# Kernel optimization log

Hardware: AMD Instinct MI355X
Metric: run time of the kernel (lower is better)

## Reference

```python
import jax, jax.numpy as jnp
import numpy as np

B, T, CNN, HW = 512, 256, 512, 7
V, H = 37, 8  # vocab_size, hidden_size


def setup_inputs() -> dict:
    key = jax.random.key(0)
    ks = jax.random.split(key, 10)
    s = 0.1
    return {
        "features": jax.random.normal(ks[0], (B, CNN, HW, HW), jnp.float32),
        "captions": jax.random.normal(ks[1], (B, T, V), jnp.float32),
        "W_in": jax.random.normal(ks[2], (V, CNN), jnp.float32) * s,
        "b_in": jax.random.normal(ks[3], (V,), jnp.float32) * s,
        "W_ih": jax.random.normal(ks[4], (4 * H, V), jnp.float32) * s,
        "W_hh": jax.random.normal(ks[5], (4 * H, H), jnp.float32) * s,
        "b_ih": jax.random.normal(ks[6], (4 * H,), jnp.float32) * s,
        "b_hh": jax.random.normal(ks[7], (4 * H,), jnp.float32) * s,
        "W_out": jax.random.normal(ks[8], (V, H), jnp.float32) * s,
        "b_out": jax.random.normal(ks[9], (V,), jnp.float32) * s,
    }


def reference(features, captions, W_in, b_in, W_ih, W_hh, b_ih, b_hh, W_out, b_out):
    # AdaptiveAvgPool2d(1) + flatten + fc_in -> [B, V]
    feat = features.mean(axis=(2, 3)) @ W_in.T + b_in
    # input at t=0 is feat, at t>0 is captions[:, t-1]; build [T, B, V] sequence
    xs = jnp.concatenate([feat[None], jnp.swapaxes(captions, 0, 1)[:-1]], axis=0)

    def step(carry, x):
        h, c = carry
        gates = x @ W_ih.T + b_ih + h @ W_hh.T + b_hh  # [B, 4H]
        i, f, g, o = jnp.split(gates, 4, axis=1)  # PyTorch LSTMCell gate order
        i = jax.nn.sigmoid(i)
        f = jax.nn.sigmoid(f)
        g = jnp.tanh(g)
        o = jax.nn.sigmoid(o)
        c = f * c + i * g
        h = o * jnp.tanh(c)
        out = jax.nn.softmax(h @ W_out.T + b_out, axis=1)  # [B, V]
        return (h, c), out

    h0 = jnp.zeros((feat.shape[0], W_hh.shape[1]), feat.dtype)
    c0 = jnp.zeros_like(h0)
    _, outs = jax.lax.scan(step, (h0, c0), xs)  # outs: [T, B, V]
    return jnp.swapaxes(outs, 0, 1)  # [B, T, V]
```

## Files before the change

### kernel.cpp

```cpp
#include <hip/hip_runtime.h>
#include <math.h>

#define BB   512
#define TT   256
#define CNNC 512
#define VV   37
#define HH   8
#define G4   32
#define CH   16
#define NCH  (TT / CH)
#define CHW  (CH * 128)

#define L2E 1.4426950408889634f

typedef float f4_t __attribute__((ext_vector_type(4)));
typedef float f2_t __attribute__((ext_vector_type(2)));

template <int CTRL>
__device__ __forceinline__ float dpp_f(float x) {
    int r = __builtin_amdgcn_update_dpp(0, __float_as_int(x), CTRL, 0xF, 0xF, true);
    return __int_as_float(r);
}

__device__ __forceinline__ float rcp_f(float x) { return __builtin_amdgcn_rcpf(x); }
__device__ __forceinline__ float exp2_f(float x) { return __builtin_amdgcn_exp2f(x); }

__global__ __launch_bounds__(256) void k_feat(const float* __restrict__ features,
                                              const float* __restrict__ W_in,
                                              const float* __restrict__ b_in,
                                              float* __restrict__ featp) {
    __shared__ __align__(16) float raw[128 * 49];
    __shared__ float pooled[128];
    const int b = blockIdx.x, qt = blockIdx.y, tid = threadIdx.x;
    const f4_t* src =
        (const f4_t*)(features + (size_t)b * CNNC * 49 + qt * (128 * 49));
    f4_t* dst = (f4_t*)raw;
    for (int i = tid; i < 128 * 49 / 4; i += 256)
        dst[i] = __builtin_nontemporal_load(&src[i]);
    __syncthreads();
    if (tid < 128) {
        const float* p = raw + tid * 49;
        float s = 0.f;
        #pragma unroll
        for (int i = 0; i < 49; ++i) s += p[i];
        pooled[tid] = s;
    }
    __syncthreads();
    const int v = tid >> 2, pp = tid & 3;
    if (v < VV) {
        const float* w = W_in + v * CNNC + qt * 128 + pp * 32;
        const float* q = pooled + pp * 32;
        float s = 0.f;
        #pragma unroll
        for (int i = 0; i < 32; ++i) s += q[i] * w[i];
        s += __shfl_xor(s, 1);
        s += __shfl_xor(s, 2);
        if (pp == 0)
            featp[(qt * BB + b) * VV + v] =
                s * (1.f / 49.f) + (qt == 0 ? b_in[v] : 0.f);
    }
}

#define CAPS 1188
#define SOS  132
__global__ __launch_bounds__(256) void k_xproj(const float* __restrict__ captions,
                                               const float* __restrict__ W_ih,
                                               const float* __restrict__ b_ih,
                                               const float* __restrict__ b_hh,
                                               const float* __restrict__ featp,
                                               float* __restrict__ xproj) {
    __shared__ float W[G4 * VV];
    __shared__ float bias[G4];
    __shared__ float cap[4 * CAPS];
    __shared__ __align__(16) float so[32 * SOS];
    const int bg = blockIdx.x, tile = blockIdx.y;
    const int tid = threadIdx.x;
    for (int i = tid; i < G4 * VV; i += 256) W[i] = W_ih[i];
    if (tid < G4) bias[tid] = b_ih[tid] + b_hh[tid];

    const int t0 = tile * 32;
    const int start = (tile == 0) ? 0 : t0 - 1;
    for (int i = tid; i < 4 * 1184; i += 256) {
        const int s2 = i / 1184;
        const int off = i - s2 * 1184;
        cap[s2 * CAPS + off] = __builtin_nontemporal_load(
            &captions[((size_t)(bg * 4 + s2) * TT + start) * VV + off]);
    }
    __syncthreads();

    const int tl = tid >> 3;
    const int s  = (tid >> 1) & 3;
    const int r  = tid & 1;
    const int b  = bg * 4 + s;

    float xr[VV];
    if (tile == 0 && tl == 0) {
        #pragma unroll
        for (int v = 0; v < VV; ++v)
            xr[v] = featp[b * VV + v] + featp[(BB + b) * VV + v] +
                    featp[(2 * BB + b) * VV + v] + featp[(3 * BB + b) * VV + v];
    } else {
        const int lr = (tile == 0) ? tl - 1 : tl;
        const float* x = &cap[s * CAPS + lr * VV];
        #pragma unroll
        for (int v = 0; v < VV; ++v) xr[v] = x[v];
    }

    const int g0 = r * 16;
    float acc[16];
    #pragma unroll
    for (int g = 0; g < 16; ++g) acc[g] = bias[g0 + g];
    #pragma unroll
    for (int v = 0; v < VV; ++v) {
        const float xv = xr[v];
        #pragma unroll
        for (int g = 0; g < 16; ++g) acc[g] += xv * W[(g0 + g) * VV + v];
    }
    #pragma unroll
    for (int g = 0; g < 16; ++g) {
        const int gg = g0 + g;
        const float sc = (gg >= 16 && gg < 24) ? (-2.f * L2E) : (-L2E);
        const int word = ((gg & 15) * 4 + s) * 2 + (gg >> 4);
        so[tl * SOS + word] = acc[g] * sc;
    }
    __syncthreads();

    float* chunk = xproj + ((size_t)bg * TT + t0) * 128;
    for (int i = tid; i < 1024; i += 256) {
        const int t2 = i >> 5, rest = i & 31;
        f4_t val = *(const f4_t*)&so[t2 * SOS + rest * 4];
        *(f4_t*)&chunk[t2 * 128 + rest * 4] = val;
    }
}

#define TSTR 12
#define SSTR (CH * TSTR + 4)

#define STEP(cur, tl) do {                                                  \
    const float pA = cur[tl].x, pB = cur[tl].y;                             \
    const float ha0 = h;                                                    \
    const float ha1 = dpp_f<0x4E>(h);                                       \
    const float ha3 = dpp_f<0x141>(h);                                      \
    const float ha2 = dpp_f<0x4E>(ha3);                                     \
    const float ha7 = dpp_f<0x140>(h);                                      \
    const float ha4 = dpp_f<0x141>(ha7);                                    \
    const float ha5 = dpp_f<0x4E>(ha4);                                     \
    const float ha6 = dpp_f<0x1B>(ha7);                                     \
    float a0 = fmaf(wA[0], ha0, pA);                                        \
    a0 = fmaf(wA[1], ha1, a0);                                              \
    a0 = fmaf(wA[2], ha2, a0);                                              \
    a0 = fmaf(wA[3], ha3, a0);                                              \
    float a1 = wA[4] * ha4;                                                 \
    a1 = fmaf(wA[5], ha5, a1);                                              \
    a1 = fmaf(wA[6], ha6, a1);                                              \
    a1 = fmaf(wA[7], ha7, a1);                                              \
    const float npA = a0 + a1;                                              \
    float b0 = fmaf(wB[0], ha0, pB);                                        \
    b0 = fmaf(wB[1], ha1, b0);                                              \
    b0 = fmaf(wB[2], ha2, b0);                                              \
    b0 = fmaf(wB[3], ha3, b0);                                              \
    float b1 = wB[4] * ha4;                                                 \
    b1 = fmaf(wB[5], ha5, b1);                                              \
    b1 = fmaf(wB[6], ha6, b1);                                              \
    b1 = fmaf(wB[7], ha7, b1);                                              \
    const float npB = b0 + b1;                                              \
    const float eA = rcp_f(1.f + exp2_f(npA));         \
    const float uB = rcp_f(1.f + exp2_f(npB));     \
    const float gg = fmaf(-4.f * L2E, uB, 2.f * L2E);    \
    const float myU = r ? eA : eA * gg;           \
    const float otU = dpp_f<0xB1>(myU);                                     \
    const float fg  = r ? myU : otU;                                        \
    const float igg = r ? otU : myU;                                        \
    const float ogx = dpp_f<0xB1>(uB);                                      \
    const float og  = r ? uB : ogx;                                         \
    c = fmaf(fg, c, igg);                         \
    const float rv = rcp_f(1.f + exp2_f(c));                                \
    const float og2 = og + og;                                              \
    h = fmaf(og2, rv, -og);                                 \
    hsv[tl] = h;                                                            \
} while (0)

#define CHUNK(cur, nxt, it, pbuf) do {                                      \
    if ((it) + 1 < NCH) {                                                   \
        const f2_t* src = (const f2_t*)(xp + ((it) + 1) * CHW + roff2);     \
        _Pragma("unroll")                                                   \
        for (int tl = 0; tl < CH; ++tl) nxt[tl] = src[tl * 64];             \
        __builtin_amdgcn_sched_barrier(0);                                  \
    }                                                                       \
    _Pragma("unroll")                                                       \
    for (int tl = 0; tl < CH; ++tl) STEP(cur, tl);                          \
    if (r == 0) {                                                           \
        float* hb = &hst[((pbuf) * 4 + s4) * SSTR + j];                     \
        _Pragma("unroll")                                                   \
        for (int i = 0; i < CH; ++i) hb[i * TSTR] = hsv[i];                 \
    }                                                                       \
} while (0)

#define EMIT(pk) do {                                                       \
    const int os = lane >> 4, otl = lane & 15;                              \
    const float* hp = &hst[(((pk) & 1) * 4 + os) * SSTR + otl * TSTR];      \
    const f4_t h0 = *(const f4_t*)hp;                                       \
    const f4_t h1 = *(const f4_t*)(hp + 4);                                 \
    const f4_t* W4 = (const f4_t*)Wo;                                       \
    float z[VV];                                                            \
    float m = -1e30f;                                                       \
    _Pragma("unroll")                                                       \
    for (int v = 0; v < VV; ++v) {                                          \
        const f4_t w0 = W4[v * 2], w1 = W4[v * 2 + 1];                      \
        float sv = bo[v];                                                   \
        sv = fmaf(h0.x, w0.x, sv); sv = fmaf(h0.y, w0.y, sv);               \
        sv = fmaf(h0.z, w0.z, sv); sv = fmaf(h0.w, w0.w, sv);               \
        sv = fmaf(h1.x, w1.x, sv); sv = fmaf(h1.y, w1.y, sv);               \
        sv = fmaf(h1.z, w1.z, sv); sv = fmaf(h1.w, w1.w, sv);               \
        z[v] = sv;                                                          \
        m = fmaxf(m, sv);                                                   \
    }                                                                       \
    float sum = 0.f;                                                        \
    _Pragma("unroll")                                                       \
    for (int v = 0; v < VV; ++v) {                                          \
        z[v] = exp2_f((z[v] - m) * L2E);                                    \
        sum += z[v];                                                        \
    }                                                                       \
    const float rs = rcp_f(sum);                                            \
    const int ob = bg * 4 + os;                                             \
    const int ot = (pk) * CH + otl;                                         \
    float* op = out + ((size_t)ob * TT + ot) * VV;                          \
    _Pragma("unroll")                                                       \
    for (int v = 0; v < VV; ++v) op[v] = z[v] * rs;                         \
} while (0)

__global__ __launch_bounds__(128) void k_lstm(const float* __restrict__ W_hh,
                                              const float* __restrict__ xproj,
                                              const float* __restrict__ W_out,
                                              const float* __restrict__ b_out,
                                              float* __restrict__ out) {
    __shared__ __align__(16) float hst[2 * 4 * SSTR];
    __shared__ __align__(16) float Wo[VV * HH];
    __shared__ float bo[VV];

    const int tid  = threadIdx.x;
    const int wv   = tid >> 6;
    const int lane = tid & 63;
    const int bg   = blockIdx.x;
    const float* xp = xproj + (size_t)bg * (TT * 128);

    const int s4 = lane >> 4;
    const int q  = lane & 15;
    const int j  = q >> 1;
    const int r  = q & 1;
    const int rowA  = r * 8 + j;
    const int roff2 = (rowA * 4 + s4) * 2;

    f2_t cA[CH], cB[CH];
    float hsv[CH];
    float wA[HH], wB[HH];

    if (wv == 0) {
        const int rowB = 16 + rowA;
        const float scA = -L2E;
        const float scB = r ? -L2E : (-2.f * L2E);
        #pragma unroll
        for (int m = 0; m < HH; ++m) {
            wA[m] = scA * W_hh[rowA * HH + (j ^ m)];
            wB[m] = scB * W_hh[rowB * HH + (j ^ m)];
        }
        const f2_t* src = (const f2_t*)(xp + roff2);
        #pragma unroll
        for (int tl = 0; tl < CH; ++tl) cA[tl] = src[tl * 64];
    } else {
        for (int i = lane; i < VV * HH; i += 64) Wo[i] = W_out[i];
        if (lane < VV) bo[lane] = b_out[lane];
    }

    float h = 0.f, c = 0.f;

    for (int ou = 0; ou < 9; ++ou) {
        {
            const int it = ou * 2;
            if (wv == 0) {
                if (it < NCH) CHUNK(cA, cB, it, 0);
            } else if (it >= 1 && it <= NCH) {
                EMIT(it - 1);
            }
            asm volatile("s_waitcnt lgkmcnt(0)" ::: "memory");
            __builtin_amdgcn_s_barrier();
            __builtin_amdgcn_sched_barrier(0);
        }
        {
            const int it = ou * 2 + 1;
            if (it <= NCH) {
                if (wv == 0) {
                    if (it < NCH) CHUNK(cB, cA, it, 1);
                } else {
                    EMIT(it - 1);
                }
                asm volatile("s_waitcnt lgkmcnt(0)" ::: "memory");
                __builtin_amdgcn_s_barrier();
                __builtin_amdgcn_sched_barrier(0);
            }
        }
    }
}

extern "C" void kernel_launch(void* const* d_in, const int* in_sizes, int n_in,
                              void* d_out, int out_size, void* d_ws, size_t ws_size,
                              hipStream_t stream) {
    const float* features = (const float*)d_in[0];
    const float* captions = (const float*)d_in[1];
    const float* W_in     = (const float*)d_in[2];
    const float* b_in     = (const float*)d_in[3];
    const float* W_ih     = (const float*)d_in[4];
    const float* W_hh     = (const float*)d_in[5];
    const float* b_ih     = (const float*)d_in[6];
    const float* b_hh     = (const float*)d_in[7];
    const float* W_out    = (const float*)d_in[8];
    const float* b_out    = (const float*)d_in[9];
    float* out = (float*)d_out;

    float* ws    = (float*)d_ws;
    float* featp = ws;
    float* xproj = ws + 81920;

    k_feat <<<dim3(BB, 4),  256, 0, stream>>>(features, W_in, b_in, featp);
    k_xproj<<<dim3(128, 8), 256, 0, stream>>>(captions, W_ih, b_ih, b_hh, featp, xproj);
    k_lstm <<<128,          128, 0, stream>>>(W_hh, xproj, W_out, b_out, out);
}
```

Baseline: 192.2 us.

## Map one LSTM hidden unit per lane with all four gates, 8 sequences per wave

The recurrent kernel now puts each hidden unit's four gates in a single lane, so no DPP exchange is needed between gate pairs. Each wave covers 8 sequences instead of 4, which halves the grid to 64 blocks and halves the chunk length. The xproj layout is rearranged so each lane reads one float4 per timestep. Softmax outputs are staged in shared memory and written with coalesced nontemporal vector stores. The trade-off is more serial arithmetic per lane on the recurrence critical path and fewer blocks to cover the GPU's compute units.

```diff
diff --git a/kernel.cpp b/kernel.cpp
--- a/kernel.cpp
+++ b/kernel.cpp
@@ -7,14 +7,13 @@
 #define VV   37
 #define HH   8
 #define G4   32
-#define CH   16
+#define CH   8
 #define NCH  (TT / CH)
-#define CHW  (CH * 128)
+#define CHW  (CH * 256)
 
 #define L2E 1.4426950408889634f
 
 typedef float f4_t __attribute__((ext_vector_type(4)));
-typedef float f2_t __attribute__((ext_vector_type(2)));
 
 template <int CTRL>
 __device__ __forceinline__ float dpp_f(float x) {
@@ -118,18 +117,20 @@
     }
     #pragma unroll
     for (int g = 0; g < 16; ++g) {
-        const int gg = g0 + g;
-        const float sc = (gg >= 16 && gg < 24) ? (-2.f * L2E) : (-L2E);
-        const int word = ((gg & 15) * 4 + s) * 2 + (gg >> 4);
+        const int gg   = g0 + g;
+        const int gate = gg >> 3;
+        const int j    = gg & 7;
+        const float sc = (gate == 2) ? (-2.f * L2E) : (-L2E);
+        const int word = s * 32 + j * 4 + gate;
         so[tl * SOS + word] = acc[g] * sc;
     }
     __syncthreads();
 
-    float* chunk = xproj + ((size_t)bg * TT + t0) * 128;
+    float* chunk = xproj + ((size_t)(bg >> 1) * TT + t0) * 256 + (bg & 1) * 128;
     for (int i = tid; i < 1024; i += 256) {
         const int t2 = i >> 5, rest = i & 31;
         f4_t val = *(const f4_t*)&so[t2 * SOS + rest * 4];
-        *(f4_t*)&chunk[t2 * 128 + rest * 4] = val;
+        *(f4_t*)&chunk[t2 * 256 + rest * 4] = val;
     }
 }
 
@@ -137,68 +138,75 @@
 #define SSTR (CH * TSTR + 4)
 
 #define STEP(cur, tl) do {                                                  \
-    const float pA = cur[tl].x, pB = cur[tl].y;                             \
+    const float pI = cur[tl].x, pF = cur[tl].y;                             \
+    const float pG = cur[tl].z, pO = cur[tl].w;                             \
     const float ha0 = h;                                                    \
-    const float ha1 = dpp_f<0x4E>(h);                                       \
-    const float ha3 = dpp_f<0x141>(h);                                      \
-    const float ha2 = dpp_f<0x4E>(ha3);                                     \
-    const float ha7 = dpp_f<0x140>(h);                                      \
-    const float ha4 = dpp_f<0x141>(ha7);                                    \
-    const float ha5 = dpp_f<0x4E>(ha4);                                     \
-    const float ha6 = dpp_f<0x1B>(ha7);                                     \
-    float a0 = fmaf(wA[0], ha0, pA);                                        \
-    a0 = fmaf(wA[1], ha1, a0);                                              \
-    a0 = fmaf(wA[2], ha2, a0);                                              \
-    a0 = fmaf(wA[3], ha3, a0);                                              \
-    float a1 = wA[4] * ha4;                                                 \
-    a1 = fmaf(wA[5], ha5, a1);                                              \
-    a1 = fmaf(wA[6], ha6, a1);                                              \
-    a1 = fmaf(wA[7], ha7, a1);                                              \
-    const float npA = a0 + a1;                                              \
-    float b0 = fmaf(wB[0], ha0, pB);                                        \
-    b0 = fmaf(wB[1], ha1, b0);                                              \
-    b0 = fmaf(wB[2], ha2, b0);                                              \
-    b0 = fmaf(wB[3], ha3, b0);                                              \
-    float b1 = wB[4] * ha4;                                                 \
-    b1 = fmaf(wB[5], ha5, b1);                                              \
-    b1 = fmaf(wB[6], ha6, b1);                                              \
-    b1 = fmaf(wB[7], ha7, b1);                                              \
-    const float npB = b0 + b1;                                              \
-    const float eA = rcp_f(1.f + exp2_f(npA));         \
-    const float uB = rcp_f(1.f + exp2_f(npB));     \
-    const float gg = fmaf(-4.f * L2E, uB, 2.f * L2E);    \
-    const float myU = r ? eA : eA * gg;           \
-    const float otU = dpp_f<0xB1>(myU);                                     \
-    const float fg  = r ? myU : otU;                                        \
-    const float igg = r ? otU : myU;                                        \
-    const float ogx = dpp_f<0xB1>(uB);                                      \
-    const float og  = r ? uB : ogx;                                         \
-    c = fmaf(fg, c, igg);                         \
+    const float ha1 = dpp_f<0xB1>(h);                                       \
+    const float ha2 = dpp_f<0x4E>(h);                                       \
+    const float ha3 = dpp_f<0x1B>(h);                                       \
+    const float ha7 = dpp_f<0x141>(h);                                      \
+    const float ha4 = dpp_f<0x1B>(ha7);                                     \
+    const float ha5 = dpp_f<0x4E>(ha7);                                     \
+    const float ha6 = dpp_f<0xB1>(ha7);                                     \
+    float iA = fmaf(wI[0], ha0, pI);                                        \
+    iA = fmaf(wI[1], ha1, iA); iA = fmaf(wI[2], ha2, iA);                   \
+    iA = fmaf(wI[3], ha3, iA);                                              \
+    float iB = wI[4] * ha4;                                                 \
+    iB = fmaf(wI[5], ha5, iB); iB = fmaf(wI[6], ha6, iB);                   \
+    iB = fmaf(wI[7], ha7, iB);                                              \
+    const float npI = iA + iB;                                              \
+    float fA = fmaf(wF[0], ha0, pF);                                        \
+    fA = fmaf(wF[1], ha1, fA); fA = fmaf(wF[2], ha2, fA);                   \
+    fA = fmaf(wF[3], ha3, fA);                                              \
+    float fB = wF[4] * ha4;                                                 \
+    fB = fmaf(wF[5], ha5, fB); fB = fmaf(wF[6], ha6, fB);                   \
+    fB = fmaf(wF[7], ha7, fB);                                              \
+    const float npF = fA + fB;                                              \
+    float gA = fmaf(wG[0], ha0, pG);                                        \
+    gA = fmaf(wG[1], ha1, gA); gA = fmaf(wG[2], ha2, gA);                   \
+    gA = fmaf(wG[3], ha3, gA);                                              \
+    float gB = wG[4] * ha4;                                                 \
+    gB = fmaf(wG[5], ha5, gB); gB = fmaf(wG[6], ha6, gB);                   \
+    gB = fmaf(wG[7], ha7, gB);                                              \
+    const float npG = gA + gB;                                              \
+    float oA = fmaf(wO[0], ha0, pO);                                        \
+    oA = fmaf(wO[1], ha1, oA); oA = fmaf(wO[2], ha2, oA);                   \
+    oA = fmaf(wO[3], ha3, oA);                                              \
+    float oB = wO[4] * ha4;                                                 \
+    oB = fmaf(wO[5], ha5, oB); oB = fmaf(wO[6], ha6, oB);                   \
+    oB = fmaf(wO[7], ha7, oB);                                              \
+    const float npO = oA + oB;                                              \
+    const float gi = rcp_f(1.f + exp2_f(npI));              \
+    const float gf = rcp_f(1.f + exp2_f(npF));              \
+    const float uG = rcp_f(1.f + exp2_f(npG));        \
+    const float go = rcp_f(1.f + exp2_f(npO));              \
+    const float gg = fmaf(-4.f * L2E, uG, 2.f * L2E);    \
+    const float ig = gi * gg;                                               \
+    c = fmaf(gf, c, ig);                          \
     const float rv = rcp_f(1.f + exp2_f(c));                                \
-    const float og2 = og + og;                                              \
-    h = fmaf(og2, rv, -og);                                 \
+    h = fmaf(go + go, rv, -go);                    \
     hsv[tl] = h;                                                            \
 } while (0)
 
 #define CHUNK(cur, nxt, it, pbuf) do {                                      \
     if ((it) + 1 < NCH) {                                                   \
-        const f2_t* src = (const f2_t*)(xp + ((it) + 1) * CHW + roff2);     \
+        const f4_t* src = (const f4_t*)(xp + (size_t)((it) + 1) * CHW);     \
         _Pragma("unroll")                                                   \
-        for (int tl = 0; tl < CH; ++tl) nxt[tl] = src[tl * 64];             \
+        for (int tl = 0; tl < CH; ++tl) nxt[tl] = src[tl * 64 + lane];      \
         __builtin_amdgcn_sched_barrier(0);                                  \
     }                                                                       \
     _Pragma("unroll")                                                       \
     for (int tl = 0; tl < CH; ++tl) STEP(cur, tl);                          \
-    if (r == 0) {                                                           \
-        float* hb = &hst[((pbuf) * 4 + s4) * SSTR + j];                     \
+    {                                                                       \
+        float* hb = &hst[((pbuf) * 8 + s8) * SSTR + j];                     \
         _Pragma("unroll")                                                   \
         for (int i = 0; i < CH; ++i) hb[i * TSTR] = hsv[i];                 \
     }                                                                       \
 } while (0)
 
 #define EMIT(pk) do {                                                       \
-    const int os = lane >> 4, otl = lane & 15;                              \
-    const float* hp = &hst[(((pk) & 1) * 4 + os) * SSTR + otl * TSTR];      \
+    const int os = lane >> 3, otl = lane & 7;                               \
+    const float* hp = &hst[(((pk) & 1) * 8 + os) * SSTR + otl * TSTR];      \
     const f4_t h0 = *(const f4_t*)hp;                                       \
     const f4_t h1 = *(const f4_t*)(hp + 4);                                 \
     const f4_t* W4 = (const f4_t*)Wo;                                       \
@@ -222,11 +230,16 @@
         sum += z[v];                                                        \
     }                                                                       \
     const float rs = rcp_f(sum);                                            \
-    const int ob = bg * 4 + os;                                             \
-    const int ot = (pk) * CH + otl;                                         \
-    float* op = out + ((size_t)ob * TT + ot) * VV;                          \
-    _Pragma("unroll")                                                       \
-    for (int v = 0; v < VV; ++v) op[v] = z[v] * rs;                         \
+    _Pragma("unroll")                                                       \
+    for (int v = 0; v < VV; ++v) zst[lane * VV + v] = z[v] * rs;            \
+                   \
+    _Pragma("unroll")                                                       \
+    for (int sq = 0; sq < 8; ++sq) {                                        \
+        const f4_t* sp = (const f4_t*)&zst[sq * (CH * VV)];                 \
+        f4_t* gp = (f4_t*)(out + ((size_t)(bg * 8 + sq) * TT + (pk) * CH) * VV); \
+        for (int k2 = lane; k2 < CH * VV / 4; k2 += 64)                     \
+            __builtin_nontemporal_store(sp[k2], &gp[k2]);                   \
+    }                                                                       \
 } while (0)
 
 __global__ __launch_bounds__(128) void k_lstm(const float* __restrict__ W_hh,
@@ -234,7 +247,8 @@
                                               const float* __restrict__ W_out,
                                               const float* __restrict__ b_out,
                                               float* __restrict__ out) {
-    __shared__ __align__(16) float hst[2 * 4 * SSTR];
+    __shared__ __align__(16) float hst[2 * 8 * SSTR];
+    __shared__ __align__(16) float zst[8 * CH * VV];
     __shared__ __align__(16) float Wo[VV * HH];
     __shared__ float bo[VV];
 
@@ -242,31 +256,26 @@
     const int wv   = tid >> 6;
     const int lane = tid & 63;
     const int bg   = blockIdx.x;
-    const float* xp = xproj + (size_t)bg * (TT * 128);
-
-    const int s4 = lane >> 4;
-    const int q  = lane & 15;
-    const int j  = q >> 1;
-    const int r  = q & 1;
-    const int rowA  = r * 8 + j;
-    const int roff2 = (rowA * 4 + s4) * 2;
-
-    f2_t cA[CH], cB[CH];
+    const float* xp = xproj + (size_t)bg * (TT * 256);
+
+    const int s8 = lane >> 3;
+    const int j  = lane & 7;
+
+    f4_t cA[CH], cB[CH];
     float hsv[CH];
-    float wA[HH], wB[HH];
+    float wI[HH], wF[HH], wG[HH], wO[HH];
 
     if (wv == 0) {
-        const int rowB = 16 + rowA;
-        const float scA = -L2E;
-        const float scB = r ? -L2E : (-2.f * L2E);
         #pragma unroll
         for (int m = 0; m < HH; ++m) {
-            wA[m] = scA * W_hh[rowA * HH + (j ^ m)];
-            wB[m] = scB * W_hh[rowB * HH + (j ^ m)];
+            wI[m] = -L2E        * W_hh[(     j) * HH + (j ^ m)];
+            wF[m] = -L2E        * W_hh[( 8 + j) * HH + (j ^ m)];
+            wG[m] = -2.f * L2E  * W_hh[(16 + j) * HH + (j ^ m)];
+            wO[m] = -L2E        * W_hh[(24 + j) * HH + (j ^ m)];
         }
-        const f2_t* src = (const f2_t*)(xp + roff2);
-        #pragma unroll
-        for (int tl = 0; tl < CH; ++tl) cA[tl] = src[tl * 64];
+        const f4_t* src = (const f4_t*)xp;
+        #pragma unroll
+        for (int tl = 0; tl < CH; ++tl) cA[tl] = src[tl * 64 + lane];
     } else {
         for (int i = lane; i < VV * HH; i += 64) Wo[i] = W_out[i];
         if (lane < VV) bo[lane] = b_out[lane];
@@ -274,7 +283,7 @@
 
     float h = 0.f, c = 0.f;
 
-    for (int ou = 0; ou < 9; ++ou) {
+    for (int ou = 0; ou < 17; ++ou) {
         {
             const int it = ou * 2;
             if (wv == 0) {
@@ -323,5 +332,5 @@
 
     k_feat <<<dim3(BB, 4),  256, 0, stream>>>(features, W_in, b_in, featp);
     k_xproj<<<dim3(128, 8), 256, 0, stream>>>(captions, W_ih, b_ih, b_hh, featp, xproj);
-    k_lstm <<<128,          128, 0, stream>>>(W_hh, xproj, W_out, b_out, out);
-}
+    k_lstm <<<64,           128, 0, stream>>>(W_hh, xproj, W_out, b_out, out);
+}
```

Result: slower. 241.7 us (+25.7%).
